# Kernel tuning notes

Measured on AMD Instinct MI355X. Metric: run time of the kernel, lower is better.

Reference implementation:

```python
import jax, jax.numpy as jnp
import numpy as np

V, D, H, B, T = 50000, 256, 512, 64, 512
FORGET_BIAS = 1.0  # TF LSTMCell default

def setup_inputs() -> dict:
    key = jax.random.key(0)
    k1, k2, k3, k4 = jax.random.split(key, 4)
    word_indices = jax.random.randint(k1, (B, T), 0, V, dtype=jnp.int32)
    num_words = jax.random.randint(k2, (B,), 1, T + 1, dtype=jnp.int32)
    # Embedding: uniform(-1, 1) per original
    W_emb = jax.random.uniform(k3, (V, D), minval=-1.0, maxval=1.0, dtype=jnp.float32)
    # TF LSTMCell: single kernel [(D+H), 4H] with gate order i, j, f, o; zero bias
    kernel = jax.random.normal(k4, (D + H, 4 * H), dtype=jnp.float32) * 0.02
    bias = jnp.zeros((4 * H,), dtype=jnp.float32)
    return {"word_indices": word_indices, "num_words": num_words,
            "W_emb": W_emb, "kernel": kernel, "bias": bias}

def reference(word_indices, num_words, W_emb, kernel, bias):
    # embedding lookup: [B, T, D]
    x = W_emb[word_indices]
    xs = jnp.swapaxes(x, 0, 1)  # [T, B, D] time-major
    ts = jnp.arange(xs.shape[0])
    c0 = jnp.zeros((word_indices.shape[0], H), dtype=x.dtype)
    h0 = jnp.zeros_like(c0)

    def step(carry, inp):
        c, h = carry
        x_t, t = inp
        gates = jnp.concatenate([x_t, h], axis=-1) @ kernel + bias  # [B, 4H]
        i, j, f, o = jnp.split(gates, 4, axis=-1)
        c_new = jax.nn.sigmoid(f + FORGET_BIAS) * c + jax.nn.sigmoid(i) * jnp.tanh(j)
        h_new = jax.nn.sigmoid(o) * jnp.tanh(c_new)
        # static_rnn sequence_length semantics: copy state through past the end
        mask = (t < num_words)[:, None]
        c = jnp.where(mask, c_new, c)
        h = jnp.where(mask, h_new, h)
        return (c, h), None

    (c_fin, h_fin), _ = jax.lax.scan(step, (c0, h0), (xs, ts))
    # TF LSTM final_state = LSTMStateTuple(c, h); stack for a single array output
    return jnp.stack([c_fin, h_fin], axis=0)  # [2, B, H]
```

## Files before the change

### kernel.cpp

```cpp
#include <hip/hip_runtime.h>
#include <stdint.h>


#define NWG     64
#define NTHR    256
#define TSTEPS  512
#define BATCH   64
#define EDIM    256
#define HID     512
#define GCOLS   2048

typedef __attribute__((ext_vector_type(8))) short short8;
typedef __attribute__((ext_vector_type(4))) float f32x4;


__device__ __forceinline__ unsigned short f2bf(float f) {
  unsigned u = __float_as_uint(f);
  unsigned r = (u + 0x7FFFu + ((u >> 16) & 1u)) >> 16;
  return (unsigned short)r;
}
__device__ __forceinline__ float sigf(float x) {
  x = fminf(fmaxf(x, -30.0f), 30.0f);
  return 1.0f / (1.0f + __expf(-x));
}
__device__ __forceinline__ float tanh_fast(float x) {
  x = fminf(fmaxf(x, -15.0f), 15.0f);
  float e = __expf(-2.0f * x);
  return (1.0f - e) / (1.0f + e);
}

__global__ void init_ws(unsigned* ws, int nwords) {
  int i = blockIdx.x * 256 + threadIdx.x;
  if (i < nwords) ws[i] = 0u;
}

__global__ void embed_k(const int* __restrict__ widx, const float* __restrict__ Wemb,
                        unsigned short* __restrict__ xb) {
  int tb = blockIdx.x;
  int t = tb >> 6, b = tb & 63;
  int wi = widx[b * TSTEPS + t];
  const float* src = Wemb + (size_t)wi * EDIM + threadIdx.x * 4;
  float4 v = *(const float4*)src;
  ushort4 o;
  o.x = f2bf(v.x); o.y = f2bf(v.y); o.z = f2bf(v.z); o.w = f2bf(v.w);
  *(ushort4*)(xb + (size_t)tb * EDIM + threadIdx.x * 4) = o;
}

__device__ __forceinline__ void cell_update(const float* g, const float* bl, int u,
                                            int t, int nw, float& c, float& h) {
  float gi = g[u]      + bl[u];
  float gj = g[8 + u]  + bl[8 + u];
  float gf = g[16 + u] + bl[16 + u];
  float go = g[24 + u] + bl[24 + u];
  float cn = sigf(gf + 1.0f) * c + sigf(gi) * tanh_fast(gj);
  float hn = sigf(go) * tanh_fast(cn);
  if (t < nw) { c = cn; h = hn; }
}

__launch_bounds__(NTHR, 1)
__global__ void lstm_persist(const int* __restrict__ num_words,
                             const int* __restrict__ widx,
                             const float* __restrict__ Wemb,
                             const float* __restrict__ Wk,
                             const float* __restrict__ bias,
                             const unsigned short* __restrict__ xb,
                             unsigned short* __restrict__ hb0,
                             unsigned short* __restrict__ hb1,
                             unsigned* flags,
                             float* __restrict__ out,
                             int has_xb)
{
  __shared__ alignas(16) short Wlds[24576];
  __shared__ float gsc[2304];
  __shared__ float blds[32];
  __shared__ alignas(16) unsigned short hst[512];

  const int tid = threadIdx.x;
  const int u0  = blockIdx.x * 8;

  for (int q = tid; q < 3072; q += NTHR) {
    int lq = q & 63;
    int kkn = q >> 6;
    int nt = (kkn >= 24) ? 1 : 0;
    int kk = kkn - nt * 24;
    int kbase = kk * 32 + ((lq >> 4) << 3);
    int n = (nt << 4) + (lq & 15);
    int gcol = ((n >> 3) << 9) + u0 + (n & 7);
    short8 v;
#pragma unroll
    for (int j = 0; j < 8; ++j)
      v[j] = (short)f2bf(Wk[(size_t)(kbase + j) * GCOLS + gcol]);
    *(short8*)&Wlds[q * 8] = v;
  }
  if (tid < 32) blds[tid] = bias[((tid >> 3) << 9) + u0 + (tid & 7)];

  const int wv   = tid >> 6;
  const int lane = tid & 63;
  const int bb   = wv * 16 + (lane & 15);
  const int kq   = (lane >> 4) << 3;

  const int b1 = tid >> 3, u1 = tid & 7;
  const int b2 = b1 + 32,  u2 = u1;
  const int nw1 = num_words[b1], nw2 = num_words[b2];
  float c1 = 0.f, h1 = 0.f, c2 = 0.f, h2 = 0.f;

  __syncthreads();

  unsigned short* hb[2] = {hb0, hb1};

  for (int t = 0; t < TSTEPS; ++t) {
    f32x4 acc0 = {0.f, 0.f, 0.f, 0.f};
    f32x4 acc1 = {0.f, 0.f, 0.f, 0.f};

    if (has_xb) {
      const unsigned short* xrow = xb + ((size_t)t * BATCH + bb) * EDIM + kq;
#pragma unroll
      for (int kk = 0; kk < 8; ++kk) {
        short8 a  = __builtin_bit_cast(short8, *(const uint4*)(xrow + kk * 32));
        short8 w0 = *(const short8*)&Wlds[((kk)      * 64 + lane) * 8];
        short8 w1 = *(const short8*)&Wlds[((24 + kk) * 64 + lane) * 8];
        acc0 = __builtin_amdgcn_mfma_f32_16x16x32_bf16(a, w0, acc0, 0, 0, 0);
        acc1 = __builtin_amdgcn_mfma_f32_16x16x32_bf16(a, w1, acc1, 0, 0, 0);
      }
    } else {
      int wi = widx[bb * TSTEPS + t];
      const float* erow = Wemb + (size_t)wi * EDIM + kq;
#pragma unroll
      for (int kk = 0; kk < 8; ++kk) {
        float4 f0 = *(const float4*)(erow + kk * 32);
        float4 f1 = *(const float4*)(erow + kk * 32 + 4);
        short8 a;
        a[0] = (short)f2bf(f0.x); a[1] = (short)f2bf(f0.y);
        a[2] = (short)f2bf(f0.z); a[3] = (short)f2bf(f0.w);
        a[4] = (short)f2bf(f1.x); a[5] = (short)f2bf(f1.y);
        a[6] = (short)f2bf(f1.z); a[7] = (short)f2bf(f1.w);
        short8 w0 = *(const short8*)&Wlds[((kk)      * 64 + lane) * 8];
        short8 w1 = *(const short8*)&Wlds[((24 + kk) * 64 + lane) * 8];
        acc0 = __builtin_amdgcn_mfma_f32_16x16x32_bf16(a, w0, acc0, 0, 0, 0);
        acc1 = __builtin_amdgcn_mfma_f32_16x16x32_bf16(a, w1, acc1, 0, 0, 0);
      }
    }

    if (t > 0) {
      if (tid < 64) {
        const unsigned* fp = flags + (tid << 5);
        const unsigned tgt = (unsigned)t;
        for (;;) {
          unsigned v;
          asm volatile("global_load_dword %0, %1, off sc0 sc1\n\t"
                       "s_waitcnt vmcnt(0)"
                       : "=v"(v) : "v"(fp));
          if (__ballot(v >= tgt) == 0xFFFFFFFFFFFFFFFFull) break;
        }
      }
      __syncthreads();
    }

    {
      const unsigned short* hrow = hb[t & 1] + bb * HID + kq;
      uint4 af[16];
#pragma unroll
      for (int kk = 0; kk < 16; ++kk)
        asm volatile("global_load_dwordx4 %0, %1, off sc0 sc1"
                     : "=v"(af[kk]) : "v"(hrow + kk * 32));
      asm volatile("s_waitcnt vmcnt(0)" ::: "memory");
#pragma unroll
      for (int kk = 0; kk < 16; ++kk) {
        short8 a  = __builtin_bit_cast(short8, af[kk]);
        short8 w0 = *(const short8*)&Wlds[((8 + kk)  * 64 + lane) * 8];
        short8 w1 = *(const short8*)&Wlds[((32 + kk) * 64 + lane) * 8];
        acc0 = __builtin_amdgcn_mfma_f32_16x16x32_bf16(a, w0, acc0, 0, 0, 0);
        acc1 = __builtin_amdgcn_mfma_f32_16x16x32_bf16(a, w1, acc1, 0, 0, 0);
      }
    }

#pragma unroll
    for (int r = 0; r < 4; ++r) {
      int row = ((lane >> 4) << 2) + r;
      gsc[wv * 576 + row * 36 + (lane & 15)]      = acc0[r];
      gsc[wv * 576 + row * 36 + 16 + (lane & 15)] = acc1[r];
    }
    __syncthreads();

    {
      const float* g = &gsc[((b1 >> 4) * 576) + ((b1 & 15) * 36)];
      cell_update(g, blds, u1, t, nw1, c1, h1);
      hst[(b1 << 3) + u1] = f2bf(h1);
    }
    {
      const float* g = &gsc[((b2 >> 4) * 576) + ((b2 & 15) * 36)];
      cell_update(g, blds, u2, t, nw2, c2, h2);
      hst[(b2 << 3) + u2] = f2bf(h2);
    }

    if (t + 1 < TSTEPS) {
      unsigned short* hw = hb[(t + 1) & 1];
      __syncthreads();
      {
        int bs = tid >> 2, p = tid & 3;
        unsigned v = *(const unsigned*)&hst[(bs << 3) + (p << 1)];
        unsigned* dst = (unsigned*)(hw + (size_t)bs * HID + u0) + p;
        asm volatile("global_store_dword %0, %1, off sc0 sc1"
                     :: "v"(dst), "v"(v) : "memory");
      }
      asm volatile("s_waitcnt vmcnt(0)" ::: "memory");
      __syncthreads();
      if (tid == 0) {
        unsigned* fa = flags + ((unsigned)blockIdx.x << 5);
        unsigned fv = (unsigned)(t + 1);
        asm volatile("global_store_dword %0, %1, off sc0 sc1"
                     :: "v"(fa), "v"(fv) : "memory");
      }
    }
  }

  out[b1 * HID + u0 + u1]         = c1;
  out[32768 + b1 * HID + u0 + u1] = h1;
  out[b2 * HID + u0 + u2]         = c2;
  out[32768 + b2 * HID + u0 + u2] = h2;
}

extern "C" void kernel_launch(void* const* d_in, const int* in_sizes, int n_in,
                              void* d_out, int out_size, void* d_ws, size_t ws_size,
                              hipStream_t stream) {
  const int*   widx = (const int*)d_in[0];
  const int*   nw   = (const int*)d_in[1];
  const float* Wemb = (const float*)d_in[2];
  const float* Wk   = (const float*)d_in[3];
  const float* bias = (const float*)d_in[4];
  float* out = (float*)d_out;
  char* ws = (char*)d_ws;

  unsigned* flags = (unsigned*)(ws + 256);
  unsigned short* hb0 = (unsigned short*)(ws + 8448);
  unsigned short* hb1 = (unsigned short*)(ws + 73984);
  unsigned short* xb  = (unsigned short*)(ws + 139520);

  size_t need = 139520ull + (size_t)TSTEPS * BATCH * EDIM * 2;
  int has_xb = (ws_size >= need) ? 1 : 0;

  size_t init_bytes = ws_size < 139520ull ? ws_size : 139520ull;
  int init_words = (int)(init_bytes / 4);
  init_ws<<<(init_words + 255) / 256, 256, 0, stream>>>((unsigned*)ws, init_words);
  if (has_xb)
    embed_k<<<TSTEPS * BATCH, 64, 0, stream>>>(widx, Wemb, xb);

  void* args[] = {(void*)&nw, (void*)&widx, (void*)&Wemb, (void*)&Wk, (void*)&bias,
                  (void*)&xb, (void*)&hb0, (void*)&hb1, (void*)&flags,
                  (void*)&out, (void*)&has_xb};
  hipLaunchCooperativeKernel((void*)lstm_persist, dim3(NWG), dim3(NTHR), args, 0, stream);
}
```

Measured before the change: 2.814 ms.

## Per-wave flags and in-register gate epilogue to remove block barriers

Replaces the block-wide step synchronisation with per-wavefront flags. Each wave polls 64 flags, one per lane, that come from the matching wave in every workgroup, and publishes its own flag once it has stored its h rows. The gate epilogue now runs in registers: lanes swap gate halves with a lane shuffle (xor 8), which drops the LDS round trip through gsc/hst and all __syncthreads in the time loop. The trade-off is that h is written as 2-byte stores instead of 4-byte ones, half the lanes sit idle during the cell math, and the init kernel now always zeroes a fixed size regardless of ws_size.

Result: faster. 2.558 ms (-9.1%).

```diff
diff --git a/kernel.cpp b/kernel.cpp
--- a/kernel.cpp
+++ b/kernel.cpp
@@ -27,6 +27,12 @@
   x = fminf(fmaxf(x, -15.0f), 15.0f);
   float e = __expf(-2.0f * x);
   return (1.0f - e) / (1.0f + e);
+}
+__device__ __forceinline__ void lstm_cell(float gi, float gj, float gf, float go,
+                                          int t, int nw, float& c, float& h) {
+  float cn = sigf(gf + 1.0f) * c + sigf(gi) * tanh_fast(gj);
+  float hn = sigf(go) * tanh_fast(cn);
+  if (t < nw) { c = cn; h = hn; }
 }
 
 __global__ void init_ws(unsigned* ws, int nwords) {
@@ -44,17 +50,6 @@
   ushort4 o;
   o.x = f2bf(v.x); o.y = f2bf(v.y); o.z = f2bf(v.z); o.w = f2bf(v.w);
   *(ushort4*)(xb + (size_t)tb * EDIM + threadIdx.x * 4) = o;
-}
-
-__device__ __forceinline__ void cell_update(const float* g, const float* bl, int u,
-                                            int t, int nw, float& c, float& h) {
-  float gi = g[u]      + bl[u];
-  float gj = g[8 + u]  + bl[8 + u];
-  float gf = g[16 + u] + bl[16 + u];
-  float go = g[24 + u] + bl[24 + u];
-  float cn = sigf(gf + 1.0f) * c + sigf(gi) * tanh_fast(gj);
-  float hn = sigf(go) * tanh_fast(cn);
-  if (t < nw) { c = cn; h = hn; }
 }
 
 __launch_bounds__(NTHR, 1)
@@ -71,12 +66,11 @@
                              int has_xb)
 {
   __shared__ alignas(16) short Wlds[24576];
-  __shared__ float gsc[2304];
-  __shared__ float blds[32];
-  __shared__ alignas(16) unsigned short hst[512];
-
-  const int tid = threadIdx.x;
-  const int u0  = blockIdx.x * 8;
+
+  const int tid  = threadIdx.x;
+  const int lane = tid & 63;
+  const int wv   = tid >> 6;
+  const int u0   = blockIdx.x * 8;
 
   for (int q = tid; q < 3072; q += NTHR) {
     int lq = q & 63;
@@ -84,29 +78,38 @@
     int nt = (kkn >= 24) ? 1 : 0;
     int kk = kkn - nt * 24;
     int kbase = kk * 32 + ((lq >> 4) << 3);
-    int n = (nt << 4) + (lq & 15);
-    int gcol = ((n >> 3) << 9) + u0 + (n & 7);
+    int nn = (nt << 4) + (lq & 15);
+    int gcol = ((nn >> 3) << 9) + u0 + (nn & 7);
     short8 v;
 #pragma unroll
     for (int j = 0; j < 8; ++j)
       v[j] = (short)f2bf(Wk[(size_t)(kbase + j) * GCOLS + gcol]);
     *(short8*)&Wlds[q * 8] = v;
   }
-  if (tid < 32) blds[tid] = bias[((tid >> 3) << 9) + u0 + (tid & 7)];
-
-  const int wv   = tid >> 6;
-  const int lane = tid & 63;
-  const int bb   = wv * 16 + (lane & 15);
-  const int kq   = (lane >> 4) << 3;
-
-  const int b1 = tid >> 3, u1 = tid & 7;
-  const int b2 = b1 + 32,  u2 = u1;
-  const int nw1 = num_words[b1], nw2 = num_words[b2];
-  float c1 = 0.f, h1 = 0.f, c2 = 0.f, h2 = 0.f;
+
+  const int n   = lane & 15;
+  const int q4  = lane >> 4;
+  const int bb  = wv * 16 + n;
+  const int kq  = q4 << 3;
+  const int un  = n & 7;
+  const bool lo = (n < 8);
+
+  float bias_g[4];
+#pragma unroll
+  for (int g = 0; g < 4; ++g) bias_g[g] = bias[g * HID + u0 + un];
+  int nw_r[4];
+#pragma unroll
+  for (int r = 0; r < 4; ++r) nw_r[r] = num_words[wv * 16 + q4 * 4 + r];
+
+  float c_r[4] = {0.f, 0.f, 0.f, 0.f};
+  float h_r[4] = {0.f, 0.f, 0.f, 0.f};
+
+  unsigned* myflag = flags + ((blockIdx.x << 2) + wv) * 32;
+  const unsigned* fp = flags + ((lane << 2) + wv) * 32;
+
+  unsigned short* hb[2] = {hb0, hb1};
 
   __syncthreads();
-
-  unsigned short* hb[2] = {hb0, hb1};
 
   for (int t = 0; t < TSTEPS; ++t) {
     f32x4 acc0 = {0.f, 0.f, 0.f, 0.f};
@@ -142,31 +145,25 @@
     }
 
     if (t > 0) {
-      if (tid < 64) {
-        const unsigned* fp = flags + (tid << 5);
-        const unsigned tgt = (unsigned)t;
-        for (;;) {
-          unsigned v;
-          asm volatile("global_load_dword %0, %1, off sc0 sc1\n\t"
-                       "s_waitcnt vmcnt(0)"
-                       : "=v"(v) : "v"(fp));
-          if (__ballot(v >= tgt) == 0xFFFFFFFFFFFFFFFFull) break;
-        }
-      }
-      __syncthreads();
-    }
-
-    {
-      const unsigned short* hrow = hb[t & 1] + bb * HID + kq;
-      uint4 af[16];
+      const unsigned tgt = (unsigned)t;
+      for (;;) {
+        unsigned v;
+        asm volatile("global_load_dword %0, %1, off sc0 sc1\n\t"
+                     "s_waitcnt vmcnt(0)" : "=v"(v) : "v"(fp));
+        if (__ballot(v >= tgt) == ~0ull) break;
+      }
+
+      const unsigned short* hr = hb[t & 1] + bb * HID + kq;
+      uint4 av[16];
 #pragma unroll
       for (int kk = 0; kk < 16; ++kk)
         asm volatile("global_load_dwordx4 %0, %1, off sc0 sc1"
-                     : "=v"(af[kk]) : "v"(hrow + kk * 32));
+                     : "=v"(av[kk]) : "v"(hr + kk * 32));
       asm volatile("s_waitcnt vmcnt(0)" ::: "memory");
+      __builtin_amdgcn_sched_barrier(0);
 #pragma unroll
       for (int kk = 0; kk < 16; ++kk) {
-        short8 a  = __builtin_bit_cast(short8, af[kk]);
+        short8 a  = __builtin_bit_cast(short8, av[kk]);
         short8 w0 = *(const short8*)&Wlds[((8 + kk)  * 64 + lane) * 8];
         short8 w1 = *(const short8*)&Wlds[((32 + kk) * 64 + lane) * 8];
         acc0 = __builtin_amdgcn_mfma_f32_16x16x32_bf16(a, w0, acc0, 0, 0, 0);
@@ -176,48 +173,45 @@
 
 #pragma unroll
     for (int r = 0; r < 4; ++r) {
-      int row = ((lane >> 4) << 2) + r;
-      gsc[wv * 576 + row * 36 + (lane & 15)]      = acc0[r];
-      gsc[wv * 576 + row * 36 + 16 + (lane & 15)] = acc1[r];
-    }
-    __syncthreads();
-
-    {
-      const float* g = &gsc[((b1 >> 4) * 576) + ((b1 & 15) * 36)];
-      cell_update(g, blds, u1, t, nw1, c1, h1);
-      hst[(b1 << 3) + u1] = f2bf(h1);
-    }
-    {
-      const float* g = &gsc[((b2 >> 4) * 576) + ((b2 & 15) * 36)];
-      cell_update(g, blds, u2, t, nw2, c2, h2);
-      hst[(b2 << 3) + u2] = f2bf(h2);
+      float a0o = acc0[r], a1o = acc1[r];
+      float a0x = __shfl_xor(a0o, 8);
+      float a1x = __shfl_xor(a1o, 8);
+      float gi = lo ? a0o : a0x;
+      float gj = lo ? a0x : a0o;
+      float gf = lo ? a1o : a1x;
+      float go = lo ? a1x : a1o;
+      lstm_cell(gi + bias_g[0], gj + bias_g[1], gf + bias_g[2], go + bias_g[3],
+                t, nw_r[r], c_r[r], h_r[r]);
     }
 
     if (t + 1 < TSTEPS) {
       unsigned short* hw = hb[(t + 1) & 1];
-      __syncthreads();
-      {
-        int bs = tid >> 2, p = tid & 3;
-        unsigned v = *(const unsigned*)&hst[(bs << 3) + (p << 1)];
-        unsigned* dst = (unsigned*)(hw + (size_t)bs * HID + u0) + p;
-        asm volatile("global_store_dword %0, %1, off sc0 sc1"
-                     :: "v"(dst), "v"(v) : "memory");
+      if (lo) {
+#pragma unroll
+        for (int r = 0; r < 4; ++r) {
+          unsigned short* dst = hw + (size_t)(wv * 16 + q4 * 4 + r) * HID + u0 + un;
+          unsigned hv = (unsigned)f2bf(h_r[r]);
+          asm volatile("global_store_short %0, %1, off sc0 sc1"
+                       :: "v"(dst), "v"(hv) : "memory");
+        }
       }
       asm volatile("s_waitcnt vmcnt(0)" ::: "memory");
-      __syncthreads();
-      if (tid == 0) {
-        unsigned* fa = flags + ((unsigned)blockIdx.x << 5);
+      if (lane == 0) {
         unsigned fv = (unsigned)(t + 1);
         asm volatile("global_store_dword %0, %1, off sc0 sc1"
-                     :: "v"(fa), "v"(fv) : "memory");
+                     :: "v"(myflag), "v"(fv) : "memory");
       }
     }
   }
 
-  out[b1 * HID + u0 + u1]         = c1;
-  out[32768 + b1 * HID + u0 + u1] = h1;
-  out[b2 * HID + u0 + u2]         = c2;
-  out[32768 + b2 * HID + u0 + u2] = h2;
+  if (lo) {
+#pragma unroll
+    for (int r = 0; r < 4; ++r) {
+      int b = wv * 16 + q4 * 4 + r;
+      out[b * HID + u0 + un]                   = c_r[r];
+      out[BATCH * HID + b * HID + u0 + un]     = h_r[r];
+    }
+  }
 }
 
 extern "C" void kernel_launch(void* const* d_in, const int* in_sizes, int n_in,
@@ -231,16 +225,15 @@
   float* out = (float*)d_out;
   char* ws = (char*)d_ws;
 
-  unsigned* flags = (unsigned*)(ws + 256);
-  unsigned short* hb0 = (unsigned short*)(ws + 8448);
-  unsigned short* hb1 = (unsigned short*)(ws + 73984);
-  unsigned short* xb  = (unsigned short*)(ws + 139520);
-
-  size_t need = 139520ull + (size_t)TSTEPS * BATCH * EDIM * 2;
+  unsigned* flags       = (unsigned*)(ws + 256);
+  unsigned short* hb0   = (unsigned short*)(ws + 33280);
+  unsigned short* hb1   = (unsigned short*)(ws + 98816);
+  unsigned short* xb    = (unsigned short*)(ws + 164352);
+
+  size_t need = 164352ull + (size_t)TSTEPS * BATCH * EDIM * 2;
   int has_xb = (ws_size >= need) ? 1 : 0;
 
-  size_t init_bytes = ws_size < 139520ull ? ws_size : 139520ull;
-  int init_words = (int)(init_bytes / 4);
+  const int init_words = 164352 / 4;
   init_ws<<<(init_words + 255) / 256, 256, 0, stream>>>((unsigned*)ws, init_words);
   if (has_xb)
     embed_k<<<TSTEPS * BATCH, 64, 0, stream>>>(widx, Wemb, xb);
```
